# Performance work log

Hardware: AMD Instinct MI355X
Metric: run time of the kernel (lower is better)

Reference implementation:

```python
import jax, jax.numpy as jnp
import numpy as np

B, N, FIN, FOUT = 8, 1024, 512, 256
ALPHA = 0.2      # LeakyReLU negative slope
EPS = 1e-5       # LayerNorm eps
NEG = -9e15      # mask value


def setup_inputs() -> dict:
    key = jax.random.key(0)
    k_h, k_adj, k_W, k_a, k_g, k_b = jax.random.split(key, 6)
    h = jax.random.normal(k_h, (B, N, FIN), dtype=jnp.float32)
    # sparse-ish binary adjacency (float, as in the torch module: adj > 0 masks)
    adj = jax.random.bernoulli(k_adj, p=0.1, shape=(B, N, N)).astype(jnp.float32)
    # xavier_uniform with gain=1.414
    def xavier(k, shape, gain=1.414):
        fan_in, fan_out = shape[0], shape[1]
        lim = gain * np.sqrt(6.0 / (fan_in + fan_out))
        return jax.random.uniform(k, shape, jnp.float32, -lim, lim)
    W = xavier(k_W, (FIN, FOUT))
    a = xavier(k_a, (2 * FOUT, 1))
    ln_gamma = jnp.ones((FOUT,), jnp.float32)
    ln_beta = jnp.zeros((FOUT,), jnp.float32)
    return {"h": h, "adj": adj, "q_type": 0, "pos": 0,
            "W": W, "a": a, "ln_gamma": ln_gamma, "ln_beta": ln_beta}


def reference(h, adj, q_type, pos, W, a, ln_gamma, ln_beta):
    # h: [B,N,FIN], adj: [B,N,N]
    Wh = jnp.einsum('bnf,fo->bno', h, W)              # [B,N,FOUT]
    # a^T [Wh_i || Wh_j] decomposes into per-node terms (same math as the
    # torch repeat/cat construction, without the [B,N,N,2F] blowup)
    a1, a2 = a[:FOUT, 0], a[FOUT:, 0]                 # [FOUT], [FOUT]
    f1 = Wh @ a1                                      # [B,N] (source i)
    f2 = Wh @ a2                                      # [B,N] (target j)
    e = jax.nn.leaky_relu(f1[:, :, None] + f2[:, None, :], negative_slope=ALPHA)
    e = jnp.where(adj > 0, e, NEG)
    attention = jax.nn.softmax(e, axis=2)             # [B,N,N]
    # dropout is a no-op at inference (training=False)
    h_prime = jnp.einsum('bij,bjo->bio', attention, Wh)  # [B,N,FOUT]
    mu = jnp.mean(h_prime, axis=-1, keepdims=True)
    var = jnp.var(h_prime, axis=-1, keepdims=True)
    h_norm = (h_prime - mu) * jax.lax.rsqrt(var + EPS) * ln_gamma + ln_beta
    return jax.nn.gelu(h_norm, approximate=False)     # concat=True -> gelu
```

## Files before the change

kernel.cpp:

```cpp
#include <hip/hip_runtime.h>
#include <math.h>

#define B_    8
#define N_    1024
#define FIN   512
#define FOUT  256
#define ALPHA 0.2f
#define EPSV  1e-5f

typedef __attribute__((ext_vector_type(8))) short bf16x8;
typedef __attribute__((ext_vector_type(4))) float f32x4;

__device__ __forceinline__ short f2bf(float x) {
    unsigned u = __builtin_bit_cast(unsigned, x);
    u = (u + 0x7FFFu + ((u >> 16) & 1u)) >> 16;
    return (short)u;
}
__device__ __forceinline__ short f2bf_fast(float x) {
    unsigned u = __builtin_bit_cast(unsigned, x);
    return (short)((u + 0x8000u) >> 16);
}
__device__ __forceinline__ float bf2f(short s) {
    return __builtin_bit_cast(float, ((unsigned)(unsigned short)s) << 16);
}
__device__ __forceinline__ float gelu_exact(float x) {
    return 0.5f * x * (1.0f + erff(x * 0.70710678118654752f));
}


__global__ __launch_bounds__(256) void k_prep(const float* __restrict__ W,
                                              short* __restrict__ WT) {
    int id  = blockIdx.x * 256 + threadIdx.x;
    int col = id >> 7;
    int k4  = (id & 127) * 4;
    short4 v;
    v.x = f2bf(W[(k4 + 0) * FOUT + col]);
    v.y = f2bf(W[(k4 + 1) * FOUT + col]);
    v.z = f2bf(W[(k4 + 2) * FOUT + col]);
    v.w = f2bf(W[(k4 + 3) * FOUT + col]);
    *(short4*)(WT + (long)col * FIN + k4) = v;
}

__global__ __launch_bounds__(256) void k_wh(const float* __restrict__ h,
                                            const short* __restrict__ WT,
                                            const float* __restrict__ a,
                                            short* __restrict__ Bpack,
                                            float* __restrict__ F1,
                                            float* __restrict__ F2) {
    const int tid = threadIdx.x;
    const int w   = tid >> 6, l = tid & 63;
    const int lr  = l & 15, lq = l >> 4;
    const long row0 = (long)blockIdx.x * 16;
    const int colbase = w * 64;

    __shared__ float r1[4][16], r2[4][16];

    f32x4 acc[4] = {};
    const float* hrow = h + (row0 + lr) * FIN + lq * 8;

    #pragma unroll
    for (int k0 = 0; k0 < FIN; k0 += 32) {
        float4 v0 = *(const float4*)(hrow + k0);
        float4 v1 = *(const float4*)(hrow + k0 + 4);
        bf16x8 af;
        af[0] = f2bf(v0.x); af[1] = f2bf(v0.y); af[2] = f2bf(v0.z); af[3] = f2bf(v0.w);
        af[4] = f2bf(v1.x); af[5] = f2bf(v1.y); af[6] = f2bf(v1.z); af[7] = f2bf(v1.w);
        #pragma unroll
        for (int c = 0; c < 4; ++c) {
            const short* bp = WT + (long)(colbase + c * 16 + lr) * FIN + k0 + lq * 8;
            bf16x8 bf = *(const bf16x8*)bp;
            acc[c] = __builtin_amdgcn_mfma_f32_16x16x32_bf16(af, bf, acc[c], 0, 0, 0);
        }
    }

    const int b   = (int)(row0 >> 10);
    const int il0 = (int)(row0 & 1023);
    const int kt  = il0 >> 5;
    const int h16 = (il0 >> 4) & 1;
    const int lp  = (h16 * 2 + (lq >> 1)) * 16 + lr;
    const int u0  = (lq & 1) * 4;
    short* bpo = Bpack + ((long)b * 16 * 32) * 512;
    #pragma unroll
    for (int c = 0; c < 4; ++c) {
        short4 s;
        s.x = f2bf(acc[c][0]); s.y = f2bf(acc[c][1]);
        s.z = f2bf(acc[c][2]); s.w = f2bf(acc[c][3]);
        int n16 = w * 4 + c;
        *(short4*)(bpo + ((long)(n16 * 32 + kt)) * 512 + lp * 8 + u0) = s;
    }

    float p1[4] = {0.f, 0.f, 0.f, 0.f}, p2[4] = {0.f, 0.f, 0.f, 0.f};
    #pragma unroll
    for (int c = 0; c < 4; ++c) {
        int col = colbase + c * 16 + lr;
        float a1v = a[col], a2v = a[FOUT + col];
        #pragma unroll
        for (int j = 0; j < 4; ++j) { p1[j] += acc[c][j] * a1v; p2[j] += acc[c][j] * a2v; }
    }
    #pragma unroll
    for (int off = 1; off < 16; off <<= 1) {
        #pragma unroll
        for (int j = 0; j < 4; ++j) {
            p1[j] += __shfl_xor(p1[j], off, 64);
            p2[j] += __shfl_xor(p2[j], off, 64);
        }
    }
    if (lr == 0) {
        #pragma unroll
        for (int j = 0; j < 4; ++j) { r1[w][lq * 4 + j] = p1[j]; r2[w][lq * 4 + j] = p2[j]; }
    }
    __syncthreads();
    if (tid < 16) {
        F1[row0 + tid] = r1[0][tid] + r1[1][tid] + r1[2][tid] + r1[3][tid];
        F2[row0 + tid] = r2[0][tid] + r2[1][tid] + r2[2][tid] + r2[3][tid];
    }
}

__global__ __launch_bounds__(256) void k_pgen(const float* __restrict__ adj,
                                              const float* __restrict__ F1,
                                              const float* __restrict__ F2,
                                              short* __restrict__ Apack) {
    const int tid = threadIdx.x;
    const int b   = blockIdx.x;
    const int m16 = blockIdx.y;
    const int ktg = blockIdx.z;
    const int w   = tid >> 6, l = tid & 63;
    const int lr  = l & 15, lq = l >> 4;
    const int i0  = m16 * 16;

    const float f1 = F1[b * N_ + i0 + lr];
    const float* __restrict__ arow = adj + ((long)b * N_ + i0 + lr) * N_;
    const float* __restrict__ f2b  = F2 + (long)b * N_;
    short* __restrict__ apb = Apack + (((long)b * 64 + m16) * 32) * 512;

    #pragma unroll
    for (int it = 0; it < 2; ++it) {
        const int kt = ktg * 8 + w * 2 + it;
        const int j0 = kt * 32 + lq * 8;
        float4 a0  = *(const float4*)(arow + j0);
        float4 a1  = *(const float4*)(arow + j0 + 4);
        float4 f20 = *(const float4*)(f2b + j0);
        float4 f21 = *(const float4*)(f2b + j0 + 4);
        float aa[8] = {a0.x, a0.y, a0.z, a0.w, a1.x, a1.y, a1.z, a1.w};
        float ff[8] = {f20.x, f20.y, f20.z, f20.w, f21.x, f21.y, f21.z, f21.w};
        bf16x8 pv;
        #pragma unroll
        for (int u = 0; u < 8; ++u) {
            float x = f1 + ff[u];
            float t = fmaxf(x, ALPHA * x);
            float e = (aa[u] > 0.f) ? __expf(t) : 0.f;
            pv[u] = f2bf_fast(e);
        }
        *(bf16x8*)(apb + (long)kt * 512 + l * 8) = pv;
    }
}

__global__ __launch_bounds__(1024, 4) void k_pv(const short* __restrict__ Apack,
                                                const short* __restrict__ Bpack,
                                                const float* __restrict__ gamma,
                                                const float* __restrict__ beta,
                                                float* __restrict__ out) {
    const int tid = threadIdx.x;
    const int b   = blockIdx.x;
    const int w   = tid >> 6, l = tid & 63;
    const int lr  = l & 15, lq = l >> 4;
    const int cw  = w & 3;
    const int rg  = (w >> 2) & 1;
    const int kg  = w >> 3;
    const int m16 = blockIdx.y * 2 + rg;

    __shared__ float sc[2][4][16][68];
    __shared__ float lnp1[2][4][16], lnp2[2][4][16];
    __shared__ float lsumS[2][2][16];

    const short* ap = Apack + (((long)b * 64 + m16) * 32 + kg * 16) * 512 + l * 8;
    const short* bp = Bpack + (((long)b * 16 + cw * 4) * 32 + kg * 16) * 512 + l * 8;

    f32x4 acc[4] = {};
    float ls = 0.f;

    bf16x8 aC  = *(const bf16x8*)ap;
    bf16x8 bC0 = *(const bf16x8*)(bp);
    bf16x8 bC1 = *(const bf16x8*)(bp + 32 * 512);
    bf16x8 bC2 = *(const bf16x8*)(bp + 64 * 512);
    bf16x8 bC3 = *(const bf16x8*)(bp + 96 * 512);

    #pragma unroll
    for (int t = 0; t < 16; ++t) {
        bf16x8 aN = aC, bN0 = bC0, bN1 = bC1, bN2 = bC2, bN3 = bC3;
        if (t < 15) {
            aN  = *(const bf16x8*)(ap + (t + 1) * 512);
            bN0 = *(const bf16x8*)(bp + (t + 1) * 512);
            bN1 = *(const bf16x8*)(bp + (32 + t + 1) * 512);
            bN2 = *(const bf16x8*)(bp + (64 + t + 1) * 512);
            bN3 = *(const bf16x8*)(bp + (96 + t + 1) * 512);
        }
        #pragma unroll
        for (int u = 0; u < 8; ++u) ls += bf2f(aC[u]);
        acc[0] = __builtin_amdgcn_mfma_f32_16x16x32_bf16(aC, bC0, acc[0], 0, 0, 0);
        acc[1] = __builtin_amdgcn_mfma_f32_16x16x32_bf16(aC, bC1, acc[1], 0, 0, 0);
        acc[2] = __builtin_amdgcn_mfma_f32_16x16x32_bf16(aC, bC2, acc[2], 0, 0, 0);
        acc[3] = __builtin_amdgcn_mfma_f32_16x16x32_bf16(aC, bC3, acc[3], 0, 0, 0);
        aC = aN; bC0 = bN0; bC1 = bN1; bC2 = bN2; bC3 = bN3;
    }

    ls += __shfl_xor(ls, 16, 64);
    ls += __shfl_xor(ls, 32, 64);
    if (cw == 0 && lq == 0) lsumS[rg][kg][lr] = ls;

    if (kg == 1) {
        #pragma unroll
        for (int cf = 0; cf < 4; ++cf)
            #pragma unroll
            for (int jj = 0; jj < 4; ++jj)
                sc[rg][cw][lq * 4 + jj][cf * 16 + lr] = acc[cf][jj];
    }
    __syncthreads();

    if (kg == 0) {
        #pragma unroll
        for (int cf = 0; cf < 4; ++cf)
            #pragma unroll
            for (int jj = 0; jj < 4; ++jj)
                acc[cf][jj] += sc[rg][cw][lq * 4 + jj][cf * 16 + lr];

        float il[4];
        #pragma unroll
        for (int jj = 0; jj < 4; ++jj) {
            float r = lsumS[rg][0][lq * 4 + jj] + lsumS[rg][1][lq * 4 + jj];
            il[jj] = (r > 0.f) ? 1.0f / r : 0.f;
        }
        float s1[4] = {0.f,0.f,0.f,0.f}, s2[4] = {0.f,0.f,0.f,0.f};
        #pragma unroll
        for (int cf = 0; cf < 4; ++cf)
            #pragma unroll
            for (int jj = 0; jj < 4; ++jj) {
                float v = acc[cf][jj] * il[jj];
                acc[cf][jj] = v;
                s1[jj] += v;
                s2[jj] += v * v;
            }
        #pragma unroll
        for (int off = 1; off < 16; off <<= 1)
            #pragma unroll
            for (int jj = 0; jj < 4; ++jj) {
                s1[jj] += __shfl_xor(s1[jj], off, 64);
                s2[jj] += __shfl_xor(s2[jj], off, 64);
            }
        if (lr == 0) {
            #pragma unroll
            for (int jj = 0; jj < 4; ++jj) {
                lnp1[rg][cw][lq * 4 + jj] = s1[jj];
                lnp2[rg][cw][lq * 4 + jj] = s2[jj];
            }
        }
    }
    __syncthreads();

    if (kg == 0) {
        #pragma unroll
        for (int jj = 0; jj < 4; ++jj) {
            int row = lq * 4 + jj;
            float t1 = lnp1[rg][0][row] + lnp1[rg][1][row] + lnp1[rg][2][row] + lnp1[rg][3][row];
            float t2 = lnp2[rg][0][row] + lnp2[rg][1][row] + lnp2[rg][2][row] + lnp2[rg][3][row];
            float mu   = t1 * (1.0f / FOUT);
            float rstd = rsqrtf(t2 * (1.0f / FOUT) - mu * mu + EPSV);
            #pragma unroll
            for (int cf = 0; cf < 4; ++cf) {
                int col = cw * 64 + cf * 16 + lr;
                out[((long)b * N_ + m16 * 16 + row) * FOUT + col] =
                    gelu_exact((acc[cf][jj] - mu) * rstd * gamma[col] + beta[col]);
            }
        }
    }
}

extern "C" void kernel_launch(void* const* d_in, const int* in_sizes, int n_in,
                              void* d_out, int out_size, void* d_ws, size_t ws_size,
                              hipStream_t stream) {
    const float* h     = (const float*)d_in[0];
    const float* adj   = (const float*)d_in[1];
    const float* W     = (const float*)d_in[4];
    const float* a     = (const float*)d_in[5];
    const float* gamma = (const float*)d_in[6];
    const float* beta  = (const float*)d_in[7];
    float* out = (float*)d_out;

    short* Apack = (short*)d_ws;
    short* Bpack = Apack + (size_t)B_ * 64 * 32 * 512;
    short* WT    = Bpack + (size_t)B_ * 16 * 32 * 512;
    float* F1    = (float*)(WT + (size_t)FOUT * FIN);
    float* F2    = F1 + (size_t)B_ * N_;

    k_prep<<<dim3(128), 256, 0, stream>>>(W, WT);
    k_wh  <<<dim3(B_ * N_ / 16), 256, 0, stream>>>(h, WT, a, Bpack, F1, F2);
    k_pgen<<<dim3(B_, N_ / 16, 4), 256, 0, stream>>>(adj, F1, F2, Apack);
    k_pv  <<<dim3(B_, N_ / 32), 1024, 0, stream>>>(Apack, Bpack, gamma, beta, out);
}
```

Before: 60.08 us.

## Fuse attention-probability generation into the PV matmul kernel

Removes the separate k_pgen kernel and its bf16 Apack workspace. The k_pv kernel now reads adj and F2 (staged in shared memory), computes the masked exp scores in registers and feeds them straight into MFMA. The block shrinks to 512 threads, with each wave covering 128 output columns (8 accumulators) instead of 64, so each score fragment is reused across more MFMAs. In exchange, B fragments are no longer software-prefetched, register pressure rises, and the exp work is repeated by both column-half waves.

```diff
diff --git a/kernel.cpp b/kernel.cpp
--- a/kernel.cpp
+++ b/kernel.cpp
@@ -116,92 +116,79 @@
     }
 }
 
-__global__ __launch_bounds__(256) void k_pgen(const float* __restrict__ adj,
-                                              const float* __restrict__ F1,
-                                              const float* __restrict__ F2,
-                                              short* __restrict__ Apack) {
-    const int tid = threadIdx.x;
-    const int b   = blockIdx.x;
-    const int m16 = blockIdx.y;
-    const int ktg = blockIdx.z;
-    const int w   = tid >> 6, l = tid & 63;
-    const int lr  = l & 15, lq = l >> 4;
-    const int i0  = m16 * 16;
-
-    const float f1 = F1[b * N_ + i0 + lr];
-    const float* __restrict__ arow = adj + ((long)b * N_ + i0 + lr) * N_;
-    const float* __restrict__ f2b  = F2 + (long)b * N_;
-    short* __restrict__ apb = Apack + (((long)b * 64 + m16) * 32) * 512;
-
-    #pragma unroll
-    for (int it = 0; it < 2; ++it) {
-        const int kt = ktg * 8 + w * 2 + it;
-        const int j0 = kt * 32 + lq * 8;
-        float4 a0  = *(const float4*)(arow + j0);
-        float4 a1  = *(const float4*)(arow + j0 + 4);
-        float4 f20 = *(const float4*)(f2b + j0);
-        float4 f21 = *(const float4*)(f2b + j0 + 4);
-        float aa[8] = {a0.x, a0.y, a0.z, a0.w, a1.x, a1.y, a1.z, a1.w};
-        float ff[8] = {f20.x, f20.y, f20.z, f20.w, f21.x, f21.y, f21.z, f21.w};
-        bf16x8 pv;
-        #pragma unroll
-        for (int u = 0; u < 8; ++u) {
-            float x = f1 + ff[u];
-            float t = fmaxf(x, ALPHA * x);
-            float e = (aa[u] > 0.f) ? __expf(t) : 0.f;
-            pv[u] = f2bf_fast(e);
-        }
-        *(bf16x8*)(apb + (long)kt * 512 + l * 8) = pv;
-    }
-}
-
-__global__ __launch_bounds__(1024, 4) void k_pv(const short* __restrict__ Apack,
-                                                const short* __restrict__ Bpack,
-                                                const float* __restrict__ gamma,
-                                                const float* __restrict__ beta,
-                                                float* __restrict__ out) {
+__global__ __launch_bounds__(512, 4) void k_pv(const short* __restrict__ Bpack,
+                                               const float* __restrict__ adj,
+                                               const float* __restrict__ F1,
+                                               const float* __restrict__ F2,
+                                               const float* __restrict__ gamma,
+                                               const float* __restrict__ beta,
+                                               float* __restrict__ out) {
     const int tid = threadIdx.x;
     const int b   = blockIdx.x;
     const int w   = tid >> 6, l = tid & 63;
     const int lr  = l & 15, lq = l >> 4;
-    const int cw  = w & 3;
-    const int rg  = (w >> 2) & 1;
-    const int kg  = w >> 3;
+    const int rg  = w >> 2;
+    const int cw  = (w >> 1) & 1;
+    const int kg  = w & 1;
     const int m16 = blockIdx.y * 2 + rg;
-
-    __shared__ float sc[2][4][16][68];
-    __shared__ float lnp1[2][4][16], lnp2[2][4][16];
+    const int i0  = m16 * 16;
+
+    __shared__ float f2s[N_];
+    __shared__ float sc[2][2][16][132];
+    __shared__ float lnp1[2][2][16], lnp2[2][2][16];
     __shared__ float lsumS[2][2][16];
 
-    const short* ap = Apack + (((long)b * 64 + m16) * 32 + kg * 16) * 512 + l * 8;
-    const short* bp = Bpack + (((long)b * 16 + cw * 4) * 32 + kg * 16) * 512 + l * 8;
-
-    f32x4 acc[4] = {};
+    { int j = tid * 2; *(float2*)&f2s[j] = *(const float2*)(F2 + b * N_ + j); }
+    __syncthreads();
+
+    const float f1 = F1[b * N_ + i0 + lr];
+    const float* __restrict__ arow = adj + ((long)b * N_ + i0 + lr) * N_;
+    const short* __restrict__ bp = Bpack + (((long)b * 16 + cw * 8) * 32 + kg * 16) * 512 + l * 8;
+    const int ktb = kg * 16;
+
+    f32x4 acc[8] = {};
     float ls = 0.f;
 
-    bf16x8 aC  = *(const bf16x8*)ap;
-    bf16x8 bC0 = *(const bf16x8*)(bp);
-    bf16x8 bC1 = *(const bf16x8*)(bp + 32 * 512);
-    bf16x8 bC2 = *(const bf16x8*)(bp + 64 * 512);
-    bf16x8 bC3 = *(const bf16x8*)(bp + 96 * 512);
+    float aa[8];
+    {
+        int j0 = ktb * 32 + lq * 8;
+        *(float4*)&aa[0] = *(const float4*)(arow + j0);
+        *(float4*)&aa[4] = *(const float4*)(arow + j0 + 4);
+    }
 
     #pragma unroll
     for (int t = 0; t < 16; ++t) {
-        bf16x8 aN = aC, bN0 = bC0, bN1 = bC1, bN2 = bC2, bN3 = bC3;
+        float aan[8];
         if (t < 15) {
-            aN  = *(const bf16x8*)(ap + (t + 1) * 512);
-            bN0 = *(const bf16x8*)(bp + (t + 1) * 512);
-            bN1 = *(const bf16x8*)(bp + (32 + t + 1) * 512);
-            bN2 = *(const bf16x8*)(bp + (64 + t + 1) * 512);
-            bN3 = *(const bf16x8*)(bp + (96 + t + 1) * 512);
-        }
-        #pragma unroll
-        for (int u = 0; u < 8; ++u) ls += bf2f(aC[u]);
-        acc[0] = __builtin_amdgcn_mfma_f32_16x16x32_bf16(aC, bC0, acc[0], 0, 0, 0);
-        acc[1] = __builtin_amdgcn_mfma_f32_16x16x32_bf16(aC, bC1, acc[1], 0, 0, 0);
-        acc[2] = __builtin_amdgcn_mfma_f32_16x16x32_bf16(aC, bC2, acc[2], 0, 0, 0);
-        acc[3] = __builtin_amdgcn_mfma_f32_16x16x32_bf16(aC, bC3, acc[3], 0, 0, 0);
-        aC = aN; bC0 = bN0; bC1 = bN1; bC2 = bN2; bC3 = bN3;
+            int j1 = (ktb + t + 1) * 32 + lq * 8;
+            *(float4*)&aan[0] = *(const float4*)(arow + j1);
+            *(float4*)&aan[4] = *(const float4*)(arow + j1 + 4);
+        }
+        const int j0 = (ktb + t) * 32 + lq * 8;
+        float f2k[8];
+        *(float4*)&f2k[0] = *(const float4*)&f2s[j0];
+        *(float4*)&f2k[4] = *(const float4*)&f2s[j0 + 4];
+
+        bf16x8 af;
+        #pragma unroll
+        for (int u = 0; u < 8; ++u) {
+            float x = f1 + f2k[u];
+            float tt = fmaxf(x, ALPHA * x);
+            float e = (aa[u] > 0.f) ? __expf(tt) : 0.f;
+            short s = f2bf_fast(e);
+            af[u] = s;
+            ls += bf2f(s);
+        }
+
+        #pragma unroll
+        for (int cf = 0; cf < 8; ++cf) {
+            bf16x8 bf = *(const bf16x8*)(bp + ((long)cf * 32 + t) * 512);
+            acc[cf] = __builtin_amdgcn_mfma_f32_16x16x32_bf16(af, bf, acc[cf], 0, 0, 0);
+        }
+        if (t < 15) {
+            #pragma unroll
+            for (int u = 0; u < 8; ++u) aa[u] = aan[u];
+        }
     }
 
     ls += __shfl_xor(ls, 16, 64);
@@ -210,7 +197,7 @@
 
     if (kg == 1) {
         #pragma unroll
-        for (int cf = 0; cf < 4; ++cf)
+        for (int cf = 0; cf < 8; ++cf)
             #pragma unroll
             for (int jj = 0; jj < 4; ++jj)
                 sc[rg][cw][lq * 4 + jj][cf * 16 + lr] = acc[cf][jj];
@@ -219,7 +206,7 @@
 
     if (kg == 0) {
         #pragma unroll
-        for (int cf = 0; cf < 4; ++cf)
+        for (int cf = 0; cf < 8; ++cf)
             #pragma unroll
             for (int jj = 0; jj < 4; ++jj)
                 acc[cf][jj] += sc[rg][cw][lq * 4 + jj][cf * 16 + lr];
@@ -232,7 +219,7 @@
         }
         float s1[4] = {0.f,0.f,0.f,0.f}, s2[4] = {0.f,0.f,0.f,0.f};
         #pragma unroll
-        for (int cf = 0; cf < 4; ++cf)
+        for (int cf = 0; cf < 8; ++cf)
             #pragma unroll
             for (int jj = 0; jj < 4; ++jj) {
                 float v = acc[cf][jj] * il[jj];
@@ -261,14 +248,14 @@
         #pragma unroll
         for (int jj = 0; jj < 4; ++jj) {
             int row = lq * 4 + jj;
-            float t1 = lnp1[rg][0][row] + lnp1[rg][1][row] + lnp1[rg][2][row] + lnp1[rg][3][row];
-            float t2 = lnp2[rg][0][row] + lnp2[rg][1][row] + lnp2[rg][2][row] + lnp2[rg][3][row];
+            float t1 = lnp1[rg][0][row] + lnp1[rg][1][row];
+            float t2 = lnp2[rg][0][row] + lnp2[rg][1][row];
             float mu   = t1 * (1.0f / FOUT);
             float rstd = rsqrtf(t2 * (1.0f / FOUT) - mu * mu + EPSV);
             #pragma unroll
-            for (int cf = 0; cf < 4; ++cf) {
-                int col = cw * 64 + cf * 16 + lr;
-                out[((long)b * N_ + m16 * 16 + row) * FOUT + col] =
+            for (int cf = 0; cf < 8; ++cf) {
+                int col = cw * 128 + cf * 16 + lr;
+                out[((long)b * N_ + i0 + row) * FOUT + col] =
                     gelu_exact((acc[cf][jj] - mu) * rstd * gamma[col] + beta[col]);
             }
         }
@@ -286,14 +273,12 @@
     const float* beta  = (const float*)d_in[7];
     float* out = (float*)d_out;
 
-    short* Apack = (short*)d_ws;
-    short* Bpack = Apack + (size_t)B_ * 64 * 32 * 512;
+    short* Bpack = (short*)d_ws;
     short* WT    = Bpack + (size_t)B_ * 16 * 32 * 512;
     float* F1    = (float*)(WT + (size_t)FOUT * FIN);
     float* F2    = F1 + (size_t)B_ * N_;
 
     k_prep<<<dim3(128), 256, 0, stream>>>(W, WT);
     k_wh  <<<dim3(B_ * N_ / 16), 256, 0, stream>>>(h, WT, a, Bpack, F1, F2);
-    k_pgen<<<dim3(B_, N_ / 16, 4), 256, 0, stream>>>(adj, F1, F2, Apack);
-    k_pv  <<<dim3(B_, N_ / 32), 1024, 0, stream>>>(Apack, Bpack, gamma, beta, out);
-}
+    k_pv  <<<dim3(B_, N_ / 32), 512, 0, stream>>>(Bpack, adj, F1, F2, gamma, beta, out);
+}
```

Measured after the change: 79.59 us. 1.32x slower.

## Pack adjacency into bitmask, stage F2 in LDS, deepen PV prefetch

Applied to the files above, without the earlier changes.

A new kernel reads the float adjacency once and writes a compact bitmask, permuted into the Apack tile order. The P-generation kernel then reads that bitmask and F2 from shared memory instead of streaming the float adjacency and F2 from global memory, so each thread covers four k-tiles with half as many blocks. Separately, the PV MFMA loop now prefetches operands two steps ahead instead of one, to hide load latency. The adjacency is still read in full by the new kernel, and the extra launch plus bitmask round-trip may cancel the savings.

```diff
diff --git a/kernel.cpp b/kernel.cpp
--- a/kernel.cpp
+++ b/kernel.cpp
@@ -41,6 +41,40 @@
     *(short4*)(WT + (long)col * FIN + k4) = v;
 }
 
+__global__ __launch_bounds__(256) void k_bits(const float* __restrict__ adj,
+                                              unsigned char* __restrict__ bits) {
+    const int tid = threadIdx.x;
+    const int w   = tid >> 6, l = tid & 63;
+    const long gr = (long)blockIdx.x * 4 + w;
+    const float* __restrict__ arow = adj + gr * N_;
+
+    unsigned b0 = 0, b1 = 0;
+    {
+        float4 x0 = *(const float4*)(arow + l * 8);
+        float4 x1 = *(const float4*)(arow + l * 8 + 4);
+        float aa[8] = {x0.x, x0.y, x0.z, x0.w, x1.x, x1.y, x1.z, x1.w};
+        #pragma unroll
+        for (int u = 0; u < 8; ++u) b0 |= (aa[u] > 0.f ? 1u : 0u) << u;
+        float4 y0 = *(const float4*)(arow + 512 + l * 8);
+        float4 y1 = *(const float4*)(arow + 512 + l * 8 + 4);
+        float bb[8] = {y0.x, y0.y, y0.z, y0.w, y1.x, y1.y, y1.z, y1.w};
+        #pragma unroll
+        for (int u = 0; u < 8; ++u) b1 |= (bb[u] > 0.f ? 1u : 0u) << u;
+    }
+    unsigned out2 = 0;
+    #pragma unroll
+    for (int k = 0; k < 2; ++k) {
+        int o   = 2 * l + k;
+        int lqd = o >> 5, ktd = o & 31;
+        int src = ((ktd & 15) << 2) | lqd;
+        unsigned v0 = __shfl(b0, src, 64);
+        unsigned v1 = __shfl(b1, src, 64);
+        unsigned v  = (ktd & 16) ? v1 : v0;
+        out2 |= (v & 0xFFu) << (8 * k);
+    }
+    *(unsigned short*)(bits + gr * 128 + l * 2) = (unsigned short)out2;
+}
+
 __global__ __launch_bounds__(256) void k_wh(const float* __restrict__ h,
                                             const short* __restrict__ WT,
                                             const float* __restrict__ a,
@@ -116,39 +150,40 @@
     }
 }
 
-__global__ __launch_bounds__(256) void k_pgen(const float* __restrict__ adj,
+__global__ __launch_bounds__(256) void k_pgen(const unsigned char* __restrict__ bits,
                                               const float* __restrict__ F1,
                                               const float* __restrict__ F2,
                                               short* __restrict__ Apack) {
     const int tid = threadIdx.x;
     const int b   = blockIdx.x;
     const int m16 = blockIdx.y;
-    const int ktg = blockIdx.z;
+    const int z   = blockIdx.z;
     const int w   = tid >> 6, l = tid & 63;
     const int lr  = l & 15, lq = l >> 4;
     const int i0  = m16 * 16;
 
+    __shared__ float f2s[N_];
+    { int j = tid * 4; *(float4*)&f2s[j] = *(const float4*)(F2 + b * N_ + j); }
+    __syncthreads();
+
     const float f1 = F1[b * N_ + i0 + lr];
-    const float* __restrict__ arow = adj + ((long)b * N_ + i0 + lr) * N_;
-    const float* __restrict__ f2b  = F2 + (long)b * N_;
+    const int kt0 = z * 16 + w * 4;
+    const unsigned bw = *(const unsigned*)(bits + ((long)(b * N_ + i0 + lr)) * 128 + lq * 32 + kt0);
     short* __restrict__ apb = Apack + (((long)b * 64 + m16) * 32) * 512;
 
     #pragma unroll
-    for (int it = 0; it < 2; ++it) {
-        const int kt = ktg * 8 + w * 2 + it;
-        const int j0 = kt * 32 + lq * 8;
-        float4 a0  = *(const float4*)(arow + j0);
-        float4 a1  = *(const float4*)(arow + j0 + 4);
-        float4 f20 = *(const float4*)(f2b + j0);
-        float4 f21 = *(const float4*)(f2b + j0 + 4);
-        float aa[8] = {a0.x, a0.y, a0.z, a0.w, a1.x, a1.y, a1.z, a1.w};
-        float ff[8] = {f20.x, f20.y, f20.z, f20.w, f21.x, f21.y, f21.z, f21.w};
+    for (int it = 0; it < 4; ++it) {
+        const int kt = kt0 + it;
+        const unsigned byte = (bw >> (it * 8)) & 0xFFu;
+        float f2k[8];
+        *(float4*)&f2k[0] = *(const float4*)&f2s[kt * 32 + lq * 8];
+        *(float4*)&f2k[4] = *(const float4*)&f2s[kt * 32 + lq * 8 + 4];
         bf16x8 pv;
         #pragma unroll
         for (int u = 0; u < 8; ++u) {
-            float x = f1 + ff[u];
-            float t = fmaxf(x, ALPHA * x);
-            float e = (aa[u] > 0.f) ? __expf(t) : 0.f;
+            float x  = f1 + f2k[u];
+            float tt = fmaxf(x, ALPHA * x);
+            float e  = ((byte >> u) & 1u) ? __expf(tt) : 0.f;
             pv[u] = f2bf_fast(e);
         }
         *(bf16x8*)(apb + (long)kt * 512 + l * 8) = pv;
@@ -179,29 +214,32 @@
     f32x4 acc[4] = {};
     float ls = 0.f;
 
-    bf16x8 aC  = *(const bf16x8*)ap;
-    bf16x8 bC0 = *(const bf16x8*)(bp);
-    bf16x8 bC1 = *(const bf16x8*)(bp + 32 * 512);
-    bf16x8 bC2 = *(const bf16x8*)(bp + 64 * 512);
-    bf16x8 bC3 = *(const bf16x8*)(bp + 96 * 512);
+    bf16x8 aP[2], bP[2][4];
+    #pragma unroll
+    for (int d = 0; d < 2; ++d) {
+        aP[d] = *(const bf16x8*)(ap + d * 512);
+        #pragma unroll
+        for (int cf = 0; cf < 4; ++cf)
+            bP[d][cf] = *(const bf16x8*)(bp + (long)(cf * 32 + d) * 512);
+    }
 
     #pragma unroll
     for (int t = 0; t < 16; ++t) {
-        bf16x8 aN = aC, bN0 = bC0, bN1 = bC1, bN2 = bC2, bN3 = bC3;
-        if (t < 15) {
-            aN  = *(const bf16x8*)(ap + (t + 1) * 512);
-            bN0 = *(const bf16x8*)(bp + (t + 1) * 512);
-            bN1 = *(const bf16x8*)(bp + (32 + t + 1) * 512);
-            bN2 = *(const bf16x8*)(bp + (64 + t + 1) * 512);
-            bN3 = *(const bf16x8*)(bp + (96 + t + 1) * 512);
+        const int cur = t & 1;
+        bf16x8 aC = aP[cur];
+        bf16x8 b0 = bP[cur][0], b1 = bP[cur][1], b2 = bP[cur][2], b3 = bP[cur][3];
+        if (t < 14) {
+            aP[cur] = *(const bf16x8*)(ap + (t + 2) * 512);
+            #pragma unroll
+            for (int cf = 0; cf < 4; ++cf)
+                bP[cur][cf] = *(const bf16x8*)(bp + (long)(cf * 32 + t + 2) * 512);
         }
         #pragma unroll
         for (int u = 0; u < 8; ++u) ls += bf2f(aC[u]);
-        acc[0] = __builtin_amdgcn_mfma_f32_16x16x32_bf16(aC, bC0, acc[0], 0, 0, 0);
-        acc[1] = __builtin_amdgcn_mfma_f32_16x16x32_bf16(aC, bC1, acc[1], 0, 0, 0);
-        acc[2] = __builtin_amdgcn_mfma_f32_16x16x32_bf16(aC, bC2, acc[2], 0, 0, 0);
-        acc[3] = __builtin_amdgcn_mfma_f32_16x16x32_bf16(aC, bC3, acc[3], 0, 0, 0);
-        aC = aN; bC0 = bN0; bC1 = bN1; bC2 = bN2; bC3 = bN3;
+        acc[0] = __builtin_amdgcn_mfma_f32_16x16x32_bf16(aC, b0, acc[0], 0, 0, 0);
+        acc[1] = __builtin_amdgcn_mfma_f32_16x16x32_bf16(aC, b1, acc[1], 0, 0, 0);
+        acc[2] = __builtin_amdgcn_mfma_f32_16x16x32_bf16(aC, b2, acc[2], 0, 0, 0);
+        acc[3] = __builtin_amdgcn_mfma_f32_16x16x32_bf16(aC, b3, acc[3], 0, 0, 0);
     }
 
     ls += __shfl_xor(ls, 16, 64);
@@ -291,9 +329,11 @@
     short* WT    = Bpack + (size_t)B_ * 16 * 32 * 512;
     float* F1    = (float*)(WT + (size_t)FOUT * FIN);
     float* F2    = F1 + (size_t)B_ * N_;
+    unsigned char* bits = (unsigned char*)(F2 + (size_t)B_ * N_);
 
     k_prep<<<dim3(128), 256, 0, stream>>>(W, WT);
+    k_bits<<<dim3(B_ * N_ / 4), 256, 0, stream>>>(adj, bits);
     k_wh  <<<dim3(B_ * N_ / 16), 256, 0, stream>>>(h, WT, a, Bpack, F1, F2);
-    k_pgen<<<dim3(B_, N_ / 16, 4), 256, 0, stream>>>(adj, F1, F2, Apack);
+    k_pgen<<<dim3(B_, N_ / 16, 2), 256, 0, stream>>>(bits, F1, F2, Apack);
     k_pv  <<<dim3(B_, N_ / 32), 1024, 0, stream>>>(Apack, Bpack, gamma, beta, out);
 }
```

Result: slower. 63.36 us (+5.5%).
